# Kernel tuning notes

Measured on AMD Instinct MI355X. Metric: run time of the kernel, lower is better.

Reference implementation:

```python
import jax, jax.numpy as jnp
import numpy as np

N = 100000  # nodes

def gcn_layer(x, W, b, src, dst, norm):
    # x: [N, Fin] -> [N, Fout]; symmetric-normalized aggregation (PyG GCNConv)
    h = x @ W                                   # linear first (no bias yet)
    msg = h[src] * norm[:, None]                # gather + edge-wise scale
    out = jax.ops.segment_sum(msg, dst, num_segments=N)  # scatter-add to targets
    return out + b

def _prep_edges(edge_index):
    # add self loops
    loops = jnp.arange(N, dtype=edge_index.dtype)
    src = jnp.concatenate([edge_index[0], loops])
    dst = jnp.concatenate([edge_index[1], loops])
    # deg computed on target nodes with unit edge weights
    deg = jax.ops.segment_sum(jnp.ones_like(dst, dtype=jnp.float32), dst, num_segments=N)
    dinv = jnp.where(deg > 0, jax.lax.rsqrt(deg), 0.0)
    norm = dinv[src] * dinv[dst]
    return src, dst, norm

def setup_inputs() -> dict:
    key = jax.random.key(0)
    ks = jax.random.split(key, 8)
    F_in, H1, H2, C = 512, 256, 64, 10
    E = 3200000
    x = jax.random.normal(ks[0], (N, F_in), dtype=jnp.float32)
    edge_index = jax.random.randint(ks[1], (2, E), 0, N, dtype=jnp.int64)
    def glorot(k, fan_in, fan_out):
        s = jnp.sqrt(6.0 / (fan_in + fan_out))
        return jax.random.uniform(k, (fan_in, fan_out), jnp.float32, -s, s)
    return {
        "x": x,
        "edge_index": edge_index,
        "W1": glorot(ks[2], F_in, H1), "b1": jnp.zeros((H1,), jnp.float32),
        "W2": glorot(ks[3], H1, H2),   "b2": jnp.zeros((H2,), jnp.float32),
        "W3": glorot(ks[4], H2, C),    "b3": jnp.zeros((C,), jnp.float32),
    }

def reference(x, edge_index, W1, b1, W2, b2, W3, b3):
    src, dst, norm = _prep_edges(edge_index)
    h = jax.nn.relu(gcn_layer(x, W1, b1, src, dst, norm))
    h = jax.nn.relu(gcn_layer(h, W2, b2, src, dst, norm))
    h = gcn_layer(h, W3, b3, src, dst, norm)
    return jax.nn.log_softmax(h, axis=1)
```

## Files before the change

kernel.cpp:

```cpp
#include <hip/hip_runtime.h>
#include <math.h>

#define NNODES 100000
#define NEDGES 3200000
#define NB 391
#define PB 512
#define CHUNK 6250

typedef __attribute__((ext_vector_type(4))) float f32x4;
typedef __attribute__((ext_vector_type(2))) float f32x2;
typedef __attribute__((ext_vector_type(8))) short bf16x8;

__device__ __forceinline__ float bf2f(ushort u) {
    union { unsigned u; float f; } v; v.u = ((unsigned)u) << 16; return v.f;
}
__device__ __forceinline__ ushort f2bf(float f) {
    union { float f; unsigned u; } v; v.f = f;
    unsigned r = v.u + 0x7FFFu + ((v.u >> 16) & 1u);
    return (ushort)(r >> 16);
}

#if __has_builtin(__builtin_amdgcn_cvt_pk_fp8_f32) && __has_builtin(__builtin_amdgcn_cvt_pk_f32_fp8)
#define FP8_HW 1
#else
#define FP8_HW 0
#endif

__device__ __forceinline__ unsigned fp8enc_sw(float f) {
    union { float f; unsigned u; } v; v.f = f;
    unsigned sign = v.u >> 31;
    float a = fabsf(f);
    if (a >= 448.0f) return (sign << 7) | 0x7E;
    if (a < 0.0009765625f) return sign << 7;
    unsigned u = v.u & 0x7FFFFFFFu;
    u += 0x7FFFFu + ((u >> 20) & 1u);
    int e2 = (int)(u >> 23) - 127;
    if (e2 < -6) {
        int m = (int)(a * 512.0f + 0.5f); if (m > 7) m = 7;
        return (sign << 7) | (unsigned)m;
    }
    if (e2 > 8) return (sign << 7) | 0x7E;
    unsigned mant = (u >> 20) & 7u;
    return (sign << 7) | ((unsigned)(e2 + 7) << 3) | mant;
}
__device__ __forceinline__ float fp8dec_sw(unsigned b) {
    unsigned s = b >> 7, e = (b >> 3) & 0xF, m = b & 7;
    float v;
    if (e == 0) v = (float)m * 0.001953125f;
    else { union { unsigned u; float f; } x; x.u = ((e + 120u) << 23) | (m << 20); v = x.f; }
    return s ? -v : v;
}

__device__ __forceinline__ unsigned char f2fp8(float f) {
#if FP8_HW
    return (unsigned char)(__builtin_amdgcn_cvt_pk_fp8_f32(f, 0.f, 0, false) & 0xFF);
#else
    return (unsigned char)fp8enc_sw(f);
#endif
}
__device__ __forceinline__ void fp8x4_acc(unsigned w, float& ax, float& ay, float& az, float& aw) {
#if FP8_HW
    f32x2 lo = __builtin_amdgcn_cvt_pk_f32_fp8((int)w, false);
    f32x2 hi = __builtin_amdgcn_cvt_pk_f32_fp8((int)w, true);
    ax += lo[0]; ay += lo[1]; az += hi[0]; aw += hi[1];
#else
    ax += fp8dec_sw(w & 0xFF); ay += fp8dec_sw((w >> 8) & 0xFF);
    az += fp8dec_sw((w >> 16) & 0xFF); aw += fp8dec_sw(w >> 24);
#endif
}

__global__ void bucket_hist(const int* __restrict__ dst, int e, int* __restrict__ hist) {
    __shared__ int h[NB];
    const int b = blockIdx.x, t = threadIdx.x;
    for (int j = t; j < NB; j += 256) h[j] = 0;
    __syncthreads();
    const int lo = b * CHUNK;
    int hi = lo + CHUNK; if (hi > e) hi = e;
    for (int i = lo + t; i < hi; i += 256)
        atomicAdd(&h[dst[i] >> 8], 1);
    __syncthreads();
    for (int j = t; j < NB; j += 256) hist[b * NB + j] = h[j];
}

__global__ void scan_buckets(int* __restrict__ hist, int* __restrict__ btotal) {
    __shared__ int s[256];
    const int j = blockIdx.x, t = threadIdx.x;
    int v0 = hist[(2 * t) * NB + j];
    int v1 = hist[(2 * t + 1) * NB + j];
    int p = v0 + v1;
    s[t] = p;
    __syncthreads();
    for (int off = 1; off < 256; off <<= 1) {
        int u = (t >= off) ? s[t - off] : 0;
        __syncthreads();
        s[t] += u;
        __syncthreads();
    }
    int excl = s[t] - p;
    hist[(2 * t) * NB + j] = excl;
    hist[(2 * t + 1) * NB + j] = excl + v0;
    if (t == 255) btotal[j] = s[255];
}

__global__ void scan_btotal(const int* __restrict__ btotal, int* __restrict__ bstart, int e) {
    __shared__ int s[512];
    const int t = threadIdx.x;
    int v = (t < NB) ? btotal[t] : 0;
    s[t] = v;
    __syncthreads();
    for (int off = 1; off < 512; off <<= 1) {
        int u = (t >= off) ? s[t - off] : 0;
        __syncthreads();
        s[t] += u;
        __syncthreads();
    }
    if (t < NB) bstart[t] = s[t] - v;
    if (t == 0) bstart[NB] = e;
}

__global__ void bucket_scatter(const int* __restrict__ src, const int* __restrict__ dst, int e,
                               const int* __restrict__ hist, const int* __restrict__ bstart,
                               unsigned* __restrict__ bucketed) {
    __shared__ int off[NB];
    const int b = blockIdx.x, t = threadIdx.x;
    for (int j = t; j < NB; j += 256) off[j] = bstart[j] + hist[b * NB + j];
    __syncthreads();
    const int lo = b * CHUNK;
    int hi = lo + CHUNK; if (hi > e) hi = e;
    for (int i = lo + t; i < hi; i += 256) {
        int d = dst[i];
        int j = d >> 8;
        int p = atomicAdd(&off[j], 1);
        bucketed[p] = (unsigned)src[i] | ((unsigned)(d & 255) << 24);
    }
}

__global__ void bucket_count_scan(const unsigned* __restrict__ bucketed, const int* __restrict__ bstart,
                                  float* __restrict__ dinv, int* __restrict__ rowptr, int n, int e) {
    __shared__ int h[256];
    __shared__ int s[256];
    const int j = blockIdx.x, t = threadIdx.x;
    h[t] = 0;
    __syncthreads();
    const int lo = bstart[j], hi = bstart[j + 1];
    for (int i = lo + t; i < hi; i += 256)
        atomicAdd(&h[bucketed[i] >> 24], 1);
    __syncthreads();
    const int c = h[t] + 1;
    s[t] = c;
    __syncthreads();
    for (int off = 1; off < 256; off <<= 1) {
        int u = (t >= off) ? s[t - off] : 0;
        __syncthreads();
        s[t] += u;
        __syncthreads();
    }
    const int excl = s[t] - c;
    const int base = j << 8;
    const int node = base + t;
    if (node < n) {
        dinv[node] = rsqrtf((float)c);
        rowptr[node] = bstart[j] + base + excl;
    }
    if (j == 0 && t == 0) rowptr[n] = e + n;
}

__global__ void fill_csr(const unsigned* __restrict__ bucketed, const int* __restrict__ bstart,
                         const int* __restrict__ rowptr, int* __restrict__ esrc, int n) {
    __shared__ int cnt[256];
    __shared__ int rp[256];
    const int j = blockIdx.x, t = threadIdx.x;
    const int base = j << 8;
    const int node = base + t;
    cnt[t] = 0;
    rp[t] = (node < n) ? rowptr[node] : 0;
    __syncthreads();
    if (node < n) esrc[rp[t]] = node;
    const int lo = bstart[j], hi = bstart[j + 1];
    for (int i = lo + t; i < hi; i += 256) {
        unsigned e = bucketed[i];
        int l = e >> 24;
        int off = atomicAdd(&cnt[l], 1);
        esrc[rp[l] + 1 + off] = (int)(e & 0xFFFFFFu);
    }
}

__global__ void conv_bf16(const float* __restrict__ x, ushort* __restrict__ xb, long n4) {
    long i = (long)blockIdx.x * blockDim.x + threadIdx.x;
    long stride = (long)gridDim.x * blockDim.x;
    for (; i < n4; i += stride) {
        float4 v = ((const float4*)x)[i];
        ushort4 o;
        o.x = f2bf(v.x); o.y = f2bf(v.y); o.z = f2bf(v.z); o.w = f2bf(v.w);
        ((ushort4*)xb)[i] = o;
    }
}

__global__ void conv_wt(const float* __restrict__ W, ushort* __restrict__ Wt,
                        int K, int N, int Npad) {
    int idx = blockIdx.x * blockDim.x + threadIdx.x;
    if (idx >= Npad * K) return;
    int n = idx / K, k = idx % K;
    Wt[idx] = (n < N) ? f2bf(W[(size_t)k * N + n]) : (ushort)0;
}

template <int BM, int BN, int BK, int WM, int WN, int OUTK>
__launch_bounds__(WM* WN * 64)
__global__ void gemm_bf16(const ushort* __restrict__ A, const ushort* __restrict__ Bt,
                          const float* __restrict__ dinv, void* __restrict__ Cout,
                          int M, int N, int K) {
    constexpr int NT = WM * WN * 64;
    __shared__ __align__(16) ushort As[BM][BK];
    __shared__ __align__(16) ushort Bs[BN][BK];
    const int tid = threadIdx.x;
    const int wid = tid >> 6, lane = tid & 63;
    const int wr = wid / WN, wc = wid % WN;
    constexpr int TM = BM / WM, TN = BN / WN;
    constexpr int FM = TM / 16, FN = TN / 16;
    const int m0 = blockIdx.y * BM, n0 = blockIdx.x * BN;
    const int ln = lane & 15, ks = (lane >> 4) * 8;

    f32x4 acc[FM][FN] = {};

    constexpr int ACH = BM * BK / 8;
    constexpr int BCH = BN * BK / 8;
    constexpr int CPR = BK / 8;

    for (int k0 = 0; k0 < K; k0 += BK) {
        #pragma unroll
        for (int it = 0; it < (ACH + NT - 1) / NT; ++it) {
            int c = it * NT + tid;
            if ((ACH % NT == 0) || (c < ACH)) {
                int row = c / CPR, ch = c % CPR;
                int gm = m0 + row; if (gm >= M) gm = M - 1;
                const ushort* gp = &A[(size_t)gm * K + k0 + ch * 8];
                __builtin_amdgcn_global_load_lds(
                    (const __attribute__((address_space(1))) void*)gp,
                    (__attribute__((address_space(3))) void*)((char*)&As[0][0] + c * 16),
                    16, 0, 0);
            }
        }
        #pragma unroll
        for (int it = 0; it < (BCH + NT - 1) / NT; ++it) {
            int c = it * NT + tid;
            if ((BCH % NT == 0) || (c < BCH)) {
                int row = c / CPR, ch = c % CPR;
                const ushort* gp = &Bt[(size_t)(n0 + row) * K + k0 + ch * 8];
                __builtin_amdgcn_global_load_lds(
                    (const __attribute__((address_space(1))) void*)gp,
                    (__attribute__((address_space(3))) void*)((char*)&Bs[0][0] + c * 16),
                    16, 0, 0);
            }
        }
        __syncthreads();

        bf16x8 af[FM], bfr[FN];
        #pragma unroll
        for (int mi = 0; mi < FM; ++mi)
            af[mi] = *(const bf16x8*)&As[wr * TM + mi * 16 + ln][ks];
        #pragma unroll
        for (int nj = 0; nj < FN; ++nj)
            bfr[nj] = *(const bf16x8*)&Bs[wc * TN + nj * 16 + ln][ks];
        #pragma unroll
        for (int mi = 0; mi < FM; ++mi)
            #pragma unroll
            for (int nj = 0; nj < FN; ++nj)
                acc[mi][nj] = __builtin_amdgcn_mfma_f32_16x16x32_bf16(af[mi], bfr[nj], acc[mi][nj], 0, 0, 0);
        __syncthreads();
    }

    const int rbase = (lane >> 4) * 4;
    #pragma unroll
    for (int mi = 0; mi < FM; ++mi) {
        #pragma unroll
        for (int r = 0; r < 4; ++r) {
            int gm = m0 + wr * TM + mi * 16 + rbase + r;
            if (gm >= M) continue;
            float d = dinv[gm];
            #pragma unroll
            for (int nj = 0; nj < FN; ++nj) {
                int gn = n0 + wc * TN + nj * 16 + ln;
                float v = acc[mi][nj][r] * d;
                if (OUTK == 1)      ((float*)Cout)[(size_t)gm * N + gn] = v;
                else if (OUTK == 0) ((ushort*)Cout)[(size_t)gm * N + gn] = f2bf(v);
                else                ((unsigned char*)Cout)[(size_t)gm * N + gn] = f2fp8(v);
            }
        }
    }
}

__global__ void agg1_fp8(const unsigned* __restrict__ h, const int* __restrict__ rowptr,
                         const int* __restrict__ esrc, const float* __restrict__ dinv,
                         const float* __restrict__ bias, ushort* __restrict__ out, int n) {
    const int wid = threadIdx.x >> 6, lane = threadIdx.x & 63;
    const int i = blockIdx.x * 4 + wid;
    if (i >= n) return;
    const int lo = rowptr[i], hi = rowptr[i + 1];
    float ax = 0.f, ay = 0.f, az = 0.f, aw = 0.f;
    int e = lo;
    for (; e + 7 < hi; e += 8) {
        int s[8];
        unsigned w[8];
        #pragma unroll
        for (int q = 0; q < 8; ++q) s[q] = esrc[e + q];
        #pragma unroll
        for (int q = 0; q < 8; ++q) w[q] = h[(size_t)s[q] * 64 + lane];
        #pragma unroll
        for (int q = 0; q < 8; ++q) fp8x4_acc(w[q], ax, ay, az, aw);
    }
    for (; e < hi; ++e)
        fp8x4_acc(h[(size_t)esrc[e] * 64 + lane], ax, ay, az, aw);

    float d = dinv[i];
    const int f0 = lane * 4;
    float4 b = *(const float4*)&bias[f0];
    ushort4 o;
    o.x = f2bf(fmaxf(ax * d + b.x, 0.f));
    o.y = f2bf(fmaxf(ay * d + b.y, 0.f));
    o.z = f2bf(fmaxf(az * d + b.z, 0.f));
    o.w = f2bf(fmaxf(aw * d + b.w, 0.f));
    *(ushort4*)&out[(size_t)i * 256 + f0] = o;
}

__global__ void agg2_kernel(const ushort* __restrict__ h, const int* __restrict__ rowptr,
                            const int* __restrict__ esrc, const float* __restrict__ dinv,
                            const float* __restrict__ bias, ushort* __restrict__ out, int n) {
    const int g = threadIdx.x >> 4, j = threadIdx.x & 15;
    const int i = blockIdx.x * 16 + g;
    if (i >= n) return;
    const int lo = rowptr[i], hi = rowptr[i + 1];
    const int f0 = j * 4;
    float ax = 0.f, ay = 0.f, az = 0.f, aw = 0.f;
    int e = lo;
    for (; e + 3 < hi; e += 4) {
        int s0 = esrc[e], s1 = esrc[e + 1], s2 = esrc[e + 2], s3 = esrc[e + 3];
        ushort4 v0 = *(const ushort4*)&h[(size_t)s0 * 64 + f0];
        ushort4 v1 = *(const ushort4*)&h[(size_t)s1 * 64 + f0];
        ushort4 v2 = *(const ushort4*)&h[(size_t)s2 * 64 + f0];
        ushort4 v3 = *(const ushort4*)&h[(size_t)s3 * 64 + f0];
        ax += bf2f(v0.x) + bf2f(v1.x) + bf2f(v2.x) + bf2f(v3.x);
        ay += bf2f(v0.y) + bf2f(v1.y) + bf2f(v2.y) + bf2f(v3.y);
        az += bf2f(v0.z) + bf2f(v1.z) + bf2f(v2.z) + bf2f(v3.z);
        aw += bf2f(v0.w) + bf2f(v1.w) + bf2f(v2.w) + bf2f(v3.w);
    }
    for (; e < hi; ++e) {
        int s = esrc[e];
        ushort4 v = *(const ushort4*)&h[(size_t)s * 64 + f0];
        ax += bf2f(v.x); ay += bf2f(v.y); az += bf2f(v.z); aw += bf2f(v.w);
    }
    float d = dinv[i];
    float4 b = *(const float4*)&bias[f0];
    ushort4 o;
    o.x = f2bf(fmaxf(ax * d + b.x, 0.f));
    o.y = f2bf(fmaxf(ay * d + b.y, 0.f));
    o.z = f2bf(fmaxf(az * d + b.z, 0.f));
    o.w = f2bf(fmaxf(aw * d + b.w, 0.f));
    *(ushort4*)&out[(size_t)i * 64 + f0] = o;
}

__global__ void agg3_logsoftmax(const float* __restrict__ h3, const int* __restrict__ rowptr,
                                const int* __restrict__ esrc, const float* __restrict__ dinv,
                                const float* __restrict__ bias, float* __restrict__ out, int n) {
    const int g = threadIdx.x >> 4, j = threadIdx.x & 15;
    const int i = blockIdx.x * 16 + g;
    if (i >= n) return;
    const int lo = rowptr[i], hi = rowptr[i + 1];
    float acc = 0.f;
    int e = lo;
    for (; e + 3 < hi; e += 4) {
        int s0 = esrc[e], s1 = esrc[e + 1], s2 = esrc[e + 2], s3 = esrc[e + 3];
        acc += h3[(size_t)s0 * 16 + j] + h3[(size_t)s1 * 16 + j]
             + h3[(size_t)s2 * 16 + j] + h3[(size_t)s3 * 16 + j];
    }
    for (; e < hi; ++e) acc += h3[(size_t)esrc[e] * 16 + j];
    float v = (j < 10) ? (acc * dinv[i] + bias[j]) : -INFINITY;
    float m = v;
    #pragma unroll
    for (int off = 1; off < 16; off <<= 1) m = fmaxf(m, __shfl_xor(m, off, 16));
    float ex = (j < 10) ? expf(v - m) : 0.f;
    float s = ex;
    #pragma unroll
    for (int off = 1; off < 16; off <<= 1) s += __shfl_xor(s, off, 16);
    if (j < 10) out[(size_t)i * 10 + j] = v - m - logf(s);
}

extern "C" void kernel_launch(void* const* d_in, const int* in_sizes, int n_in,
                              void* d_out, int out_size, void* d_ws, size_t ws_size,
                              hipStream_t stream) {
    const int N = NNODES, E = NEDGES;
    const float* x  = (const float*)d_in[0];
    const int*   ei = (const int*)d_in[1];
    const float* W1 = (const float*)d_in[2];
    const float* b1 = (const float*)d_in[3];
    const float* W2 = (const float*)d_in[4];
    const float* b2 = (const float*)d_in[5];
    const float* W3 = (const float*)d_in[6];
    const float* b3 = (const float*)d_in[7];
    float* out = (float*)d_out;
    const int* src = ei;
    const int* dst = ei + E;

    char* ws = (char*)d_ws;
    size_t off = 0;
    auto alloc = [&](size_t bytes) -> void* {
        void* p = ws + off;
        off = (off + bytes + 255) & ~(size_t)255;
        return p;
    };
    float* dinv   = (float*)alloc((size_t)N * 4);
    int*   rowptr = (int*)alloc((size_t)(N + 1) * 4);
    int*   btotal = (int*)alloc((size_t)NB * 4);
    int*   bstart = (int*)alloc((size_t)(NB + 1) * 4);
    int*   esrc   = (int*)alloc((size_t)(E + N) * 4);
    ushort* xb    = (ushort*)alloc((size_t)N * 512 * 2);
    ushort* W1t   = (ushort*)alloc((size_t)256 * 512 * 2);
    ushort* W2t   = (ushort*)alloc((size_t)64 * 256 * 2);
    ushort* W3t   = (ushort*)alloc((size_t)16 * 64 * 2);
    ushort* buf1  = (ushort*)alloc((size_t)N * 256 * 2);
    ushort* buf2  = (ushort*)alloc((size_t)N * 256 * 2);
    float* h3f    = (float*)xb;
    int*   hist   = (int*)buf1;
    unsigned* bucketed = (unsigned*)buf2;
    unsigned char* h1fp8 = (unsigned char*)buf1;

    const int T = 256;
    bucket_hist<<<PB, T, 0, stream>>>(dst, E, hist);
    scan_buckets<<<NB, T, 0, stream>>>(hist, btotal);
    scan_btotal<<<1, 512, 0, stream>>>(btotal, bstart, E);
    bucket_scatter<<<PB, T, 0, stream>>>(src, dst, E, hist, bstart, bucketed);
    bucket_count_scan<<<NB, T, 0, stream>>>(bucketed, bstart, dinv, rowptr, N, E);
    fill_csr<<<NB, T, 0, stream>>>(bucketed, bstart, rowptr, esrc, N);

    conv_bf16<<<2048, T, 0, stream>>>(x, xb, (long)N * 512 / 4);
    conv_wt<<<(256 * 512 + T - 1) / T, T, 0, stream>>>(W1, W1t, 512, 256, 256);
    conv_wt<<<(64 * 256 + T - 1) / T, T, 0, stream>>>(W2, W2t, 256, 64, 64);
    conv_wt<<<(16 * 64 + T - 1) / T, T, 0, stream>>>(W3, W3t, 64, 10, 16);

    const int MB = (N + 127) / 128;

    gemm_bf16<128, 128, 32, 2, 2, 2><<<dim3(2, MB), 256, 0, stream>>>(xb, W1t, dinv, h1fp8, N, 256, 512);
    agg1_fp8<<<(N + 3) / 4, 256, 0, stream>>>((const unsigned*)h1fp8, rowptr, esrc, dinv, b1, buf2, N);

    gemm_bf16<128, 64, 32, 2, 2, 0><<<dim3(1, MB), 256, 0, stream>>>(buf2, W2t, dinv, buf1, N, 64, 256);
    agg2_kernel<<<(N + 15) / 16, 256, 0, stream>>>(buf1, rowptr, esrc, dinv, b2, buf2, N);

    gemm_bf16<128, 16, 32, 4, 1, 1><<<dim3(1, MB), 256, 0, stream>>>(buf2, W3t, dinv, h3f, N, 16, 64);
    agg3_logsoftmax<<<(N + 15) / 16, 256, 0, stream>>>(h3f, rowptr, esrc, dinv, b3, out, N);
}
```

Baseline: 459.0 us.

## Use fp8 for layer-2 features, bf16 for layer-3, merge CSR finalize kernels

Layer-2 GEMM output is stored as fp8 and gathered with the existing fp8 accumulate helper, and layer-3 output is stored as bf16 instead of fp32, with the log-softmax kernel reworked to 8 lanes per node handling two features each. The count/scan and CSR fill kernels are merged into one, which saves a launch and a reread of rowptr. The aim is to cut gather bandwidth in the aggregation passes, at the cost of lower precision in the intermediate activations.

```diff
diff --git a/kernel.cpp b/kernel.cpp
--- a/kernel.cpp
+++ b/kernel.cpp
@@ -135,10 +135,12 @@
     }
 }
 
-__global__ void bucket_count_scan(const unsigned* __restrict__ bucketed, const int* __restrict__ bstart,
-                                  float* __restrict__ dinv, int* __restrict__ rowptr, int n, int e) {
+__global__ void bucket_finalize(const unsigned* __restrict__ bucketed, const int* __restrict__ bstart,
+                                float* __restrict__ dinv, int* __restrict__ rowptr,
+                                int* __restrict__ esrc, int n, int e) {
     __shared__ int h[256];
     __shared__ int s[256];
+    __shared__ int rp[256];
     const int j = blockIdx.x, t = threadIdx.x;
     h[t] = 0;
     __syncthreads();
@@ -158,30 +160,21 @@
     const int excl = s[t] - c;
     const int base = j << 8;
     const int node = base + t;
+    const int myrp = bstart[j] + base + excl;
+    rp[t] = myrp;
     if (node < n) {
         dinv[node] = rsqrtf((float)c);
-        rowptr[node] = bstart[j] + base + excl;
+        rowptr[node] = myrp;
+        esrc[myrp] = node;
     }
     if (j == 0 && t == 0) rowptr[n] = e + n;
-}
-
-__global__ void fill_csr(const unsigned* __restrict__ bucketed, const int* __restrict__ bstart,
-                         const int* __restrict__ rowptr, int* __restrict__ esrc, int n) {
-    __shared__ int cnt[256];
-    __shared__ int rp[256];
-    const int j = blockIdx.x, t = threadIdx.x;
-    const int base = j << 8;
-    const int node = base + t;
-    cnt[t] = 0;
-    rp[t] = (node < n) ? rowptr[node] : 0;
-    __syncthreads();
-    if (node < n) esrc[rp[t]] = node;
-    const int lo = bstart[j], hi = bstart[j + 1];
+    h[t] = 0;
+    __syncthreads();
     for (int i = lo + t; i < hi; i += 256) {
-        unsigned e = bucketed[i];
-        int l = e >> 24;
-        int off = atomicAdd(&cnt[l], 1);
-        esrc[rp[l] + 1 + off] = (int)(e & 0xFFFFFFu);
+        unsigned ed = bucketed[i];
+        int l = ed >> 24;
+        int off = atomicAdd(&h[l], 1);
+        esrc[rp[l] + 1 + off] = (int)(ed & 0xFFFFFFu);
     }
 }
 
@@ -322,33 +315,31 @@
     *(ushort4*)&out[(size_t)i * 256 + f0] = o;
 }
 
-__global__ void agg2_kernel(const ushort* __restrict__ h, const int* __restrict__ rowptr,
-                            const int* __restrict__ esrc, const float* __restrict__ dinv,
-                            const float* __restrict__ bias, ushort* __restrict__ out, int n) {
+__global__ void agg2_fp8(const unsigned* __restrict__ h, const int* __restrict__ rowptr,
+                         const int* __restrict__ esrc, const float* __restrict__ dinv,
+                         const float* __restrict__ bias, ushort* __restrict__ out, int n) {
     const int g = threadIdx.x >> 4, j = threadIdx.x & 15;
     const int i = blockIdx.x * 16 + g;
     if (i >= n) return;
     const int lo = rowptr[i], hi = rowptr[i + 1];
-    const int f0 = j * 4;
     float ax = 0.f, ay = 0.f, az = 0.f, aw = 0.f;
     int e = lo;
     for (; e + 3 < hi; e += 4) {
         int s0 = esrc[e], s1 = esrc[e + 1], s2 = esrc[e + 2], s3 = esrc[e + 3];
-        ushort4 v0 = *(const ushort4*)&h[(size_t)s0 * 64 + f0];
-        ushort4 v1 = *(const ushort4*)&h[(size_t)s1 * 64 + f0];
-        ushort4 v2 = *(const ushort4*)&h[(size_t)s2 * 64 + f0];
-        ushort4 v3 = *(const ushort4*)&h[(size_t)s3 * 64 + f0];
-        ax += bf2f(v0.x) + bf2f(v1.x) + bf2f(v2.x) + bf2f(v3.x);
-        ay += bf2f(v0.y) + bf2f(v1.y) + bf2f(v2.y) + bf2f(v3.y);
-        az += bf2f(v0.z) + bf2f(v1.z) + bf2f(v2.z) + bf2f(v3.z);
-        aw += bf2f(v0.w) + bf2f(v1.w) + bf2f(v2.w) + bf2f(v3.w);
-    }
-    for (; e < hi; ++e) {
-        int s = esrc[e];
-        ushort4 v = *(const ushort4*)&h[(size_t)s * 64 + f0];
-        ax += bf2f(v.x); ay += bf2f(v.y); az += bf2f(v.z); aw += bf2f(v.w);
-    }
+        unsigned w0 = h[(size_t)s0 * 16 + j];
+        unsigned w1 = h[(size_t)s1 * 16 + j];
+        unsigned w2 = h[(size_t)s2 * 16 + j];
+        unsigned w3 = h[(size_t)s3 * 16 + j];
+        fp8x4_acc(w0, ax, ay, az, aw);
+        fp8x4_acc(w1, ax, ay, az, aw);
+        fp8x4_acc(w2, ax, ay, az, aw);
+        fp8x4_acc(w3, ax, ay, az, aw);
+    }
+    for (; e < hi; ++e)
+        fp8x4_acc(h[(size_t)esrc[e] * 16 + j], ax, ay, az, aw);
+
     float d = dinv[i];
+    const int f0 = j * 4;
     float4 b = *(const float4*)&bias[f0];
     ushort4 o;
     o.x = f2bf(fmaxf(ax * d + b.x, 0.f));
@@ -358,30 +349,44 @@
     *(ushort4*)&out[(size_t)i * 64 + f0] = o;
 }
 
-__global__ void agg3_logsoftmax(const float* __restrict__ h3, const int* __restrict__ rowptr,
+__global__ void agg3_logsoftmax(const ushort* __restrict__ h3, const int* __restrict__ rowptr,
                                 const int* __restrict__ esrc, const float* __restrict__ dinv,
                                 const float* __restrict__ bias, float* __restrict__ out, int n) {
-    const int g = threadIdx.x >> 4, j = threadIdx.x & 15;
-    const int i = blockIdx.x * 16 + g;
+    const int g = threadIdx.x >> 3, j = threadIdx.x & 7;
+    const int i = blockIdx.x * 32 + g;
     if (i >= n) return;
     const int lo = rowptr[i], hi = rowptr[i + 1];
-    float acc = 0.f;
+    float a0 = 0.f, a1 = 0.f;
     int e = lo;
     for (; e + 3 < hi; e += 4) {
         int s0 = esrc[e], s1 = esrc[e + 1], s2 = esrc[e + 2], s3 = esrc[e + 3];
-        acc += h3[(size_t)s0 * 16 + j] + h3[(size_t)s1 * 16 + j]
-             + h3[(size_t)s2 * 16 + j] + h3[(size_t)s3 * 16 + j];
-    }
-    for (; e < hi; ++e) acc += h3[(size_t)esrc[e] * 16 + j];
-    float v = (j < 10) ? (acc * dinv[i] + bias[j]) : -INFINITY;
-    float m = v;
+        unsigned w0 = *(const unsigned*)&h3[(size_t)s0 * 16 + 2 * j];
+        unsigned w1 = *(const unsigned*)&h3[(size_t)s1 * 16 + 2 * j];
+        unsigned w2 = *(const unsigned*)&h3[(size_t)s2 * 16 + 2 * j];
+        unsigned w3 = *(const unsigned*)&h3[(size_t)s3 * 16 + 2 * j];
+        a0 += bf2f((ushort)(w0 & 0xFFFF)) + bf2f((ushort)(w1 & 0xFFFF))
+            + bf2f((ushort)(w2 & 0xFFFF)) + bf2f((ushort)(w3 & 0xFFFF));
+        a1 += bf2f((ushort)(w0 >> 16)) + bf2f((ushort)(w1 >> 16))
+            + bf2f((ushort)(w2 >> 16)) + bf2f((ushort)(w3 >> 16));
+    }
+    for (; e < hi; ++e) {
+        unsigned w = *(const unsigned*)&h3[(size_t)esrc[e] * 16 + 2 * j];
+        a0 += bf2f((ushort)(w & 0xFFFF));
+        a1 += bf2f((ushort)(w >> 16));
+    }
+    const int f0 = 2 * j;
+    float d = dinv[i];
+    float v0 = (f0 < 10) ? (a0 * d + bias[f0]) : -INFINITY;
+    float v1 = (f0 + 1 < 10) ? (a1 * d + bias[f0 + 1]) : -INFINITY;
+    float m = fmaxf(v0, v1);
     #pragma unroll
-    for (int off = 1; off < 16; off <<= 1) m = fmaxf(m, __shfl_xor(m, off, 16));
-    float ex = (j < 10) ? expf(v - m) : 0.f;
-    float s = ex;
+    for (int off = 1; off < 8; off <<= 1) m = fmaxf(m, __shfl_xor(m, off, 8));
+    float ex = ((f0 < 10) ? expf(v0 - m) : 0.f) + ((f0 + 1 < 10) ? expf(v1 - m) : 0.f);
     #pragma unroll
-    for (int off = 1; off < 16; off <<= 1) s += __shfl_xor(s, off, 16);
-    if (j < 10) out[(size_t)i * 10 + j] = v - m - logf(s);
+    for (int off = 1; off < 8; off <<= 1) ex += __shfl_xor(ex, off, 8);
+    float ls = logf(ex);
+    if (f0 < 10)     out[(size_t)i * 10 + f0] = v0 - m - ls;
+    if (f0 + 1 < 10) out[(size_t)i * 10 + f0 + 1] = v1 - m - ls;
 }
 
 extern "C" void kernel_launch(void* const* d_in, const int* in_sizes, int n_in,
@@ -418,18 +423,18 @@
     ushort* W3t   = (ushort*)alloc((size_t)16 * 64 * 2);
     ushort* buf1  = (ushort*)alloc((size_t)N * 256 * 2);
     ushort* buf2  = (ushort*)alloc((size_t)N * 256 * 2);
-    float* h3f    = (float*)xb;
     int*   hist   = (int*)buf1;
     unsigned* bucketed = (unsigned*)buf2;
     unsigned char* h1fp8 = (unsigned char*)buf1;
+    unsigned char* h2fp8 = (unsigned char*)buf1;
+    ushort* h3b   = (ushort*)xb;
 
     const int T = 256;
     bucket_hist<<<PB, T, 0, stream>>>(dst, E, hist);
     scan_buckets<<<NB, T, 0, stream>>>(hist, btotal);
     scan_btotal<<<1, 512, 0, stream>>>(btotal, bstart, E);
     bucket_scatter<<<PB, T, 0, stream>>>(src, dst, E, hist, bstart, bucketed);
-    bucket_count_scan<<<NB, T, 0, stream>>>(bucketed, bstart, dinv, rowptr, N, E);
-    fill_csr<<<NB, T, 0, stream>>>(bucketed, bstart, rowptr, esrc, N);
+    bucket_finalize<<<NB, T, 0, stream>>>(bucketed, bstart, dinv, rowptr, esrc, N, E);
 
     conv_bf16<<<2048, T, 0, stream>>>(x, xb, (long)N * 512 / 4);
     conv_wt<<<(256 * 512 + T - 1) / T, T, 0, stream>>>(W1, W1t, 512, 256, 256);
@@ -441,9 +446,9 @@
     gemm_bf16<128, 128, 32, 2, 2, 2><<<dim3(2, MB), 256, 0, stream>>>(xb, W1t, dinv, h1fp8, N, 256, 512);
     agg1_fp8<<<(N + 3) / 4, 256, 0, stream>>>((const unsigned*)h1fp8, rowptr, esrc, dinv, b1, buf2, N);
 
-    gemm_bf16<128, 64, 32, 2, 2, 0><<<dim3(1, MB), 256, 0, stream>>>(buf2, W2t, dinv, buf1, N, 64, 256);
-    agg2_kernel<<<(N + 15) / 16, 256, 0, stream>>>(buf1, rowptr, esrc, dinv, b2, buf2, N);
-
-    gemm_bf16<128, 16, 32, 4, 1, 1><<<dim3(1, MB), 256, 0, stream>>>(buf2, W3t, dinv, h3f, N, 16, 64);
-    agg3_logsoftmax<<<(N + 15) / 16, 256, 0, stream>>>(h3f, rowptr, esrc, dinv, b3, out, N);
-}
+    gemm_bf16<128, 64, 32, 2, 2, 2><<<dim3(1, MB), 256, 0, stream>>>(buf2, W2t, dinv, h2fp8, N, 64, 256);
+    agg2_fp8<<<(N + 15) / 16, 256, 0, stream>>>((const unsigned*)h2fp8, rowptr, esrc, dinv, b2, buf2, N);
+
+    gemm_bf16<128, 16, 32, 4, 1, 0><<<dim3(1, MB), 256, 0, stream>>>(buf2, W3t, dinv, h3b, N, 16, 64);
+    agg3_logsoftmax<<<(N + 31) / 32, 256, 0, stream>>>(h3b, rowptr, esrc, dinv, b3, out, N);
+}
```

New measurement: 429.2 us. 6.5% less time.
